# Performance work log

Measured on AMD Instinct MI355X. Metric: run time of the kernel, lower is better.

Reference implementation:

```python
import jax, jax.numpy as jnp
import numpy as np

B, S, H = 2, 2048, 2048
N = 16               # num heads
NOPE, ROPE, V = 128, 64, 128
QHD = NOPE + ROPE    # 192 per-head q/k dim
QL, KVL = 1536, 512  # q_lora_rank, kv_lora_rank
THETA = 10000.0
SCALE = QHD ** -0.5
EPS = 1e-6


def rmsnorm(x, w):
    var = jnp.mean(x.astype(jnp.float32) ** 2, axis=-1, keepdims=True)
    return (x.astype(jnp.float32) * jax.lax.rsqrt(var + EPS)).astype(x.dtype) * w


def rotate_half(x):
    d = x.shape[-1] // 2
    return jnp.concatenate([-x[..., d:], x[..., :d]], axis=-1)


def setup_inputs() -> dict:
    key = jax.random.key(0)
    ks = jax.random.split(key, 8)
    w = lambda k, shape: jax.random.normal(k, shape, jnp.float32) * 0.02
    return {
        "hidden_states": jax.random.normal(ks[0], (B, S, H), jnp.float32),
        "position_ids": (jnp.arange(B * S, dtype=jnp.int64) % 4096).reshape(B, S),
        "q_a_w": w(ks[1], (QL, H)),
        "q_a_ln_w": jnp.ones((QL,), jnp.float32),
        "q_b_w": w(ks[2], (N * QHD, QL)),
        "kv_a_w": w(ks[3], (KVL + ROPE, H)),
        "kv_a_ln_w": jnp.ones((KVL,), jnp.float32),
        "kv_b_w": w(ks[4], (N * (NOPE + V), KVL)),
        "o_w": w(ks[5], (H, N * V)),
    }


def mla_forward(hidden_states, position_ids, q_a_w, q_a_ln_w, q_b_w,
                kv_a_w, kv_a_ln_w, kv_b_w, o_w):
    b, s, _ = hidden_states.shape
    # ---- Q low-rank path: q_b(rmsnorm(q_a(x))) ----
    q = rmsnorm(hidden_states @ q_a_w.T, q_a_ln_w) @ q_b_w.T
    q = q.reshape(b, s, N, QHD)
    q_nope, q_pe = q[..., :NOPE], q[..., NOPE:]
    # ---- compressed KV + shared rope key ----
    kv_a = hidden_states @ kv_a_w.T                       # [b,s,KVL+ROPE]
    compressed_kv = rmsnorm(kv_a[..., :KVL], kv_a_ln_w)   # [b,s,KVL]
    k_pe = kv_a[..., KVL:].reshape(b, s, 1, ROPE)         # MQA rope key
    # ---- RoPE (default, theta=1e4) from position_ids ----
    inv_freq = 1.0 / (THETA ** (jnp.arange(0, ROPE, 2, dtype=jnp.float32) / ROPE))
    freqs = position_ids.astype(jnp.float32)[..., None] * inv_freq  # [b,s,ROPE/2]
    emb = jnp.concatenate([freqs, freqs], axis=-1)                  # [b,s,ROPE]
    cos = jnp.cos(emb)[:, :, None, :].astype(hidden_states.dtype)   # [b,s,1,ROPE]
    sin = jnp.sin(emb)[:, :, None, :].astype(hidden_states.dtype)
    q_pe = q_pe * cos + rotate_half(q_pe) * sin
    k_pe = k_pe * cos + rotate_half(k_pe) * sin
    # ---- decompress latent KV via kv_b_proj ----
    kv = (compressed_kv @ kv_b_w.T).reshape(b, s, N, NOPE + V)
    k_nope, v = kv[..., :NOPE], kv[..., NOPE:]
    k = jnp.concatenate([k_nope, jnp.broadcast_to(k_pe, (b, s, N, ROPE))], axis=-1)
    qf = jnp.concatenate([q_nope, q_pe], axis=-1)          # [b,s,N,QHD]
    # ---- causal SDPA in bsnd layout ----
    scores = jnp.einsum('bqnd,bknd->bnqk', qf, k) * SCALE  # [b,N,s,s]
    causal = jnp.tril(jnp.ones((s, s), bool))
    scores = jnp.where(causal, scores, jnp.finfo(scores.dtype).min)
    probs = jax.nn.softmax(scores, axis=-1)
    attn = jnp.einsum('bnqk,bknd->bqnd', probs, v)         # [b,s,N,V]
    out = attn.reshape(b, s, N * V) @ o_w.T
    return out


def reference(hidden_states, position_ids, q_a_w, q_a_ln_w, q_b_w,
              kv_a_w, kv_a_ln_w, kv_b_w, o_w):
    return mla_forward(hidden_states, position_ids, q_a_w, q_a_ln_w, q_b_w,
                       kv_a_w, kv_a_ln_w, kv_b_w, o_w)
```

## Files before the change

### kernel.cpp

```cpp
#include <hip/hip_runtime.h>
#include <cstdio>

typedef unsigned short u16;
typedef u16 u16x4 __attribute__((ext_vector_type(4)));
typedef u16 u16x8 __attribute__((ext_vector_type(8)));
typedef __bf16 bf16x8 __attribute__((ext_vector_type(8)));
typedef float f32x4 __attribute__((ext_vector_type(4)));

#define AS1 __attribute__((address_space(1)))
#define AS3 __attribute__((address_space(3)))

#define GLOAD16(gsrc, ldst) __builtin_amdgcn_global_load_lds( \
    (const AS1 void*)(gsrc), (AS3 void*)(ldst), 16, 0, 0)

__device__ __forceinline__ u16 f2bf(float f) {
  unsigned u = __builtin_bit_cast(unsigned, f);
  u += 0x7fffu + ((u >> 16) & 1u);
  return (u16)(u >> 16);
}
__device__ __forceinline__ float bf2f(u16 h) {
  return __builtin_bit_cast(float, (unsigned)h << 16);
}

__global__ __launch_bounds__(256) void cvt_pad_k(const float* __restrict__ src,
                                                 u16* __restrict__ dst,
                                                 long srcN, long dstN) {
  long i = ((long)blockIdx.x * 256 + threadIdx.x) * 8;
  const long stride = (long)gridDim.x * 256 * 8;
  for (; i < dstN; i += stride) {
    u16x8 o = {0,0,0,0,0,0,0,0};
    if (i < srcN) {
      const float4* p = (const float4*)(src + i);
      float4 a = p[0], b = p[1];
      o[0]=f2bf(a.x); o[1]=f2bf(a.y); o[2]=f2bf(a.z); o[3]=f2bf(a.w);
      o[4]=f2bf(b.x); o[5]=f2bf(b.y); o[6]=f2bf(b.z); o[7]=f2bf(b.w);
    }
    *(u16x8*)(dst + i) = o;
  }
}

__global__ __launch_bounds__(256) void rms_k(const u16* __restrict__ src, u16* __restrict__ dst,
                                             const float* __restrict__ w,
                                             int sstride, int dstride, int cols) {
  const int row = blockIdx.x;
  const int tid = threadIdx.x;
  const int nch = cols >> 3;
  float x[8];
  float ss = 0.f;
  if (tid < nch) {
    u16x8 v = *(const u16x8*)(src + (size_t)row * sstride + tid * 8);
#pragma unroll
    for (int j = 0; j < 8; ++j) { x[j] = bf2f(v[j]); ss += x[j] * x[j]; }
  } else {
#pragma unroll
    for (int j = 0; j < 8; ++j) x[j] = 0.f;
  }
#pragma unroll
  for (int off = 1; off < 64; off <<= 1) ss += __shfl_xor(ss, off);
  __shared__ float red[4];
  const int wv = tid >> 6, ln = tid & 63;
  if (ln == 0) red[wv] = ss;
  __syncthreads();
  const float tot = red[0] + red[1] + red[2] + red[3];
  const float rs = 1.0f / sqrtf(tot / (float)cols + 1e-6f);
  if (tid < nch) {
    u16x8 o;
#pragma unroll
    for (int j = 0; j < 8; ++j) o[j] = f2bf(x[j] * rs * w[tid * 8 + j]);
    *(u16x8*)(dst + (size_t)row * dstride + tid * 8) = o;
  }
}

__global__ __launch_bounds__(256) void rope_k(u16* __restrict__ q, const u16* __restrict__ kva,
                                              u16* __restrict__ kpe, const int* __restrict__ pos) {
  const int tok = blockIdx.x;
  const int j = threadIdx.x & 63;
  const int w = threadIdx.x >> 6;
  const float p = (float)pos[tok];
  const int jj = j & 31;
  const float inv = __powf(10000.0f, -(float)jj * (1.0f / 32.0f));
  float s, c;
  __sincosf(p * inv, &s, &c);
  const float sgn = (j < 32) ? -1.0f : 1.0f;
  const int partner = (j < 32) ? j + 32 : j - 32;
  if (w == 0) {
    const float x  = bf2f(kva[(size_t)tok * 640 + 512 + j]);
    const float xp = bf2f(kva[(size_t)tok * 640 + 512 + partner]);
    kpe[(size_t)tok * 64 + j] = f2bf(x * c + sgn * xp * s);
  }
#pragma unroll
  for (int hh = 0; hh < 4; ++hh) {
    const int h = w * 4 + hh;
    const size_t base = (size_t)tok * 3072 + h * 192 + 128;
    const float x  = bf2f(q[base + j]);
    const float xp = bf2f(q[base + partner]);
    q[base + j] = f2bf(x * c + sgn * xp * s);
  }
}

__global__ __launch_bounds__(256) void gemm_bt(const u16* __restrict__ A, const u16* __restrict__ B,
                                               u16* __restrict__ Cb, float* __restrict__ Cf,
                                               int M, int N, int K) {
  __shared__ __attribute__((aligned(16))) u16 As[128 * 64];
  __shared__ __attribute__((aligned(16))) u16 Bs[128 * 64];
  const int tid = threadIdx.x;
  const int m0 = blockIdx.y * 128, n0 = blockIdx.x * 128;
  const int w = tid >> 6, lane = tid & 63;
  const int wr = w >> 1, wc = w & 1;
  const int lr = lane & 15, g = lane >> 4;

  f32x4 acc[4][4] = {};

  for (int k0 = 0; k0 < K; k0 += 64) {
#pragma unroll
    for (int i = 0; i < 4; ++i) {
      const int c = i * 256 + tid;
      const int row = c >> 3, col = (c & 7) << 3;
      GLOAD16(A + (size_t)(m0 + row) * K + k0 + col, &As[c * 8]);
    }
#pragma unroll
    for (int i = 0; i < 4; ++i) {
      const int c = i * 256 + tid;
      const int row = c >> 3, col = (c & 7) << 3;
      GLOAD16(B + (size_t)(n0 + row) * K + k0 + col, &Bs[c * 8]);
    }
    __syncthreads();
    bf16x8 af[4][2], bfr[4][2];
#pragma unroll
    for (int x = 0; x < 4; ++x)
#pragma unroll
      for (int kk = 0; kk < 2; ++kk) {
        af[x][kk]  = *(const bf16x8*)(&As[(wr * 64 + x * 16 + lr) * 64 + kk * 32 + g * 8]);
        bfr[x][kk] = *(const bf16x8*)(&Bs[(wc * 64 + x * 16 + lr) * 64 + kk * 32 + g * 8]);
      }
#pragma unroll
    for (int mi = 0; mi < 4; ++mi)
#pragma unroll
      for (int ni = 0; ni < 4; ++ni)
#pragma unroll
        for (int kk = 0; kk < 2; ++kk)
          acc[mi][ni] = __builtin_amdgcn_mfma_f32_16x16x32_bf16(af[mi][kk], bfr[ni][kk],
                                                                acc[mi][ni], 0, 0, 0);
    __syncthreads();
  }

  const int rb = m0 + wr * 64, cb = n0 + wc * 64;
#pragma unroll
  for (int mi = 0; mi < 4; ++mi)
#pragma unroll
    for (int ni = 0; ni < 4; ++ni)
#pragma unroll
      for (int i = 0; i < 4; ++i) {
        const int r = rb + mi * 16 + g * 4 + i;
        const int cI = cb + ni * 16 + lr;
        if (Cf) Cf[(size_t)r * N + cI] = acc[mi][ni][i];
        else    Cb[(size_t)r * N + cI] = f2bf(acc[mi][ni][i]);
      }
}

__global__ __launch_bounds__(256) void attn_k(const u16* __restrict__ q, const u16* __restrict__ kvb,
                                              const u16* __restrict__ kpe, u16* __restrict__ ao) {
  __shared__ __attribute__((aligned(16))) u16 Ks[64 * 192];
  __shared__ __attribute__((aligned(16))) u16 Vt[128 * 64];
  __shared__ __attribute__((aligned(16))) u16 Ps[4][32 * 72];

  const float SCALE = 0.07216878364870323f;
  const int bh = blockIdx.x;
  const int b = bh >> 4, h = bh & 15;
  const int by = blockIdx.y;
  const int j = (by < 8) ? (15 - by) : (by - 8);
  const int tid = threadIdx.x, w = tid >> 6, lane = tid & 63;
  const int lr = lane & 15, g = lane >> 4;

  const int q0 = j * 128;
  const int qrb = q0 + w * 32;

  bf16x8 qf[2][6];
#pragma unroll
  for (int m = 0; m < 2; ++m)
#pragma unroll
    for (int kd = 0; kd < 6; ++kd)
      qf[m][kd] = *(const bf16x8*)(q + (size_t)(b * 2048 + qrb + m * 16 + lr) * 3072 +
                                   h * 192 + kd * 32 + g * 8);

  float mrow[2][4], lrow[2][4];
  f32x4 o[2][8] = {};
#pragma unroll
  for (int m = 0; m < 2; ++m)
#pragma unroll
    for (int i = 0; i < 4; ++i) { mrow[m][i] = -1e30f; lrow[m][i] = 0.f; }

  const int nt = (q0 >> 6) + 2;
  for (int t = 0; t < nt; ++t) {
    const int k0 = t * 64;
#pragma unroll
    for (int i = 0; i < 6; ++i) {
      const int c = i * 256 + tid;
      const int row = c / 24, cl = c - row * 24;
      const int cg = cl ^ (row & 7);
      const u16* src = (cg < 16)
        ? (kvb + (size_t)(b * 2048 + k0 + row) * 4096 + h * 256 + cg * 8)
        : (kpe + (size_t)(b * 2048 + k0 + row) * 64 + (cg - 16) * 8);
      GLOAD16(src, &Ks[c * 8]);
    }
    {
      const int kq = tid >> 4;
      const int vc = (tid & 15) << 3;
      u16x8 vv[4];
#pragma unroll
      for (int r = 0; r < 4; ++r)
        vv[r] = *(const u16x8*)(kvb + (size_t)(b * 2048 + k0 + kq * 4 + r) * 4096 + h * 256 + 128 + vc);
#pragma unroll
      for (int e = 0; e < 8; ++e) {
        const int v = vc + e;
        const int cx = (kq >> 1) ^ (v & 7) ^ ((v >> 3) & 7);
        u16x4 tq = {vv[0][e], vv[1][e], vv[2][e], vv[3][e]};
        *(u16x4*)(&Vt[v * 64 + cx * 8 + (kq & 1) * 4]) = tq;
      }
    }
    __syncthreads();

    if (k0 <= qrb + 31) {
      f32x4 sAcc[2][4] = {};
#pragma unroll
      for (int nf = 0; nf < 4; ++nf) {
        const int rr = nf * 16 + lr;
#pragma unroll
        for (int kd = 0; kd < 6; ++kd) {
          const int ch = (kd * 4 + g) ^ (rr & 7);
          const bf16x8 kf = *(const bf16x8*)(&Ks[rr * 192 + ch * 8]);
#pragma unroll
          for (int m = 0; m < 2; ++m)
            sAcc[m][nf] = __builtin_amdgcn_mfma_f32_16x16x32_bf16(qf[m][kd], kf, sAcc[m][nf], 0, 0, 0);
        }
      }

#pragma unroll
      for (int m = 0; m < 2; ++m) {
        float sv[4][4];
#pragma unroll
        for (int nf = 0; nf < 4; ++nf)
#pragma unroll
          for (int i = 0; i < 4; ++i) {
            const int qrow = qrb + m * 16 + g * 4 + i;
            const int kcol = k0 + nf * 16 + lr;
            const float vS = sAcc[m][nf][i] * SCALE;
            sv[nf][i] = (kcol > qrow) ? -1e30f : vS;
          }
        float rm4[4];
        bool exceed = false;
#pragma unroll
        for (int i = 0; i < 4; ++i) {
          float rm = fmaxf(fmaxf(sv[0][i], sv[1][i]), fmaxf(sv[2][i], sv[3][i]));
          rm = fmaxf(rm, __shfl_xor(rm, 1));
          rm = fmaxf(rm, __shfl_xor(rm, 2));
          rm = fmaxf(rm, __shfl_xor(rm, 4));
          rm = fmaxf(rm, __shfl_xor(rm, 8));
          rm4[i] = rm;
          exceed = exceed || (rm > mrow[m][i] + 8.0f);
        }
        if (__any(exceed)) {
#pragma unroll
          for (int i = 0; i < 4; ++i) {
            const float mn = fmaxf(mrow[m][i], rm4[i]);
            const float fac = __expf(mrow[m][i] - mn);
            mrow[m][i] = mn;
            lrow[m][i] *= fac;
#pragma unroll
            for (int nv = 0; nv < 8; ++nv) o[m][nv][i] *= fac;
          }
        }
#pragma unroll
        for (int i = 0; i < 4; ++i) {
          float rsum = 0.f;
#pragma unroll
          for (int nf = 0; nf < 4; ++nf) { sv[nf][i] = __expf(sv[nf][i] - mrow[m][i]); rsum += sv[nf][i]; }
          rsum += __shfl_xor(rsum, 1);
          rsum += __shfl_xor(rsum, 2);
          rsum += __shfl_xor(rsum, 4);
          rsum += __shfl_xor(rsum, 8);
          lrow[m][i] += rsum;
        }
#pragma unroll
        for (int nf = 0; nf < 4; ++nf)
#pragma unroll
          for (int i = 0; i < 4; ++i)
            Ps[w][(m * 16 + g * 4 + i) * 72 + nf * 16 + lr] = f2bf(sv[nf][i]);
      }
      asm volatile("s_waitcnt lgkmcnt(0)" ::: "memory");

#pragma unroll
      for (int kc = 0; kc < 2; ++kc) {
        bf16x8 vfr[8];
#pragma unroll
        for (int nv = 0; nv < 8; ++nv) {
          const int v = nv * 16 + lr;
          const int cx = (kc * 4 + g) ^ (v & 7) ^ ((v >> 3) & 7);
          vfr[nv] = *(const bf16x8*)(&Vt[v * 64 + cx * 8]);
        }
#pragma unroll
        for (int m = 0; m < 2; ++m) {
          const bf16x8 pf = *(const bf16x8*)(&Ps[w][(m * 16 + lr) * 72 + kc * 32 + g * 8]);
#pragma unroll
          for (int nv = 0; nv < 8; ++nv)
            o[m][nv] = __builtin_amdgcn_mfma_f32_16x16x32_bf16(pf, vfr[nv], o[m][nv], 0, 0, 0);
        }
      }
    }
    __syncthreads();
  }

#pragma unroll
  for (int m = 0; m < 2; ++m)
#pragma unroll
    for (int i = 0; i < 4; ++i) {
      const float inv = 1.0f / lrow[m][i];
      const size_t tokOff = (size_t)(b * 2048 + qrb + m * 16 + g * 4 + i) * 2048 + h * 128;
#pragma unroll
      for (int nv = 0; nv < 8; ++nv)
        ao[tokOff + nv * 16 + lr] = f2bf(o[m][nv][i] * inv);
    }
}

extern "C" void kernel_launch(void* const* d_in, const int* in_sizes, int n_in,
                              void* d_out, int out_size, void* d_ws, size_t ws_size,
                              hipStream_t stream) {
  const float* hidden  = (const float*)d_in[0];
  const int*   pos     = (const int*)d_in[1];
  const float* q_a_w   = (const float*)d_in[2];
  const float* q_a_ln  = (const float*)d_in[3];
  const float* q_b_w   = (const float*)d_in[4];
  const float* kv_a_w  = (const float*)d_in[5];
  const float* kv_a_ln = (const float*)d_in[6];
  const float* kv_b_w  = (const float*)d_in[7];
  const float* o_w     = (const float*)d_in[8];
  float* out = (float*)d_out;

  char* ws = (char*)d_ws;
  u16* hb  = (u16*)(ws + 0L);
  u16* w1  = (u16*)(ws + 16777216L);
  u16* w2  = (u16*)(ws + 23068672L);
  u16* w3  = (u16*)(ws + 32505856L);
  u16* w4  = (u16*)(ws + 35127296L);
  u16* w5  = (u16*)(ws + 39321600L);
  u16* qa  = (u16*)(ws + 47710208L);
  u16* qb  = (u16*)(ws + 60293120L);
  u16* kva = (u16*)(ws + 85458944L);
  u16* ckv = (u16*)(ws + 90701824L);
  u16* kpe = (u16*)(ws + 94896128L);
  u16* kvb = (u16*)(ws + 95420416L);
  u16* ao  = (u16*)(ws + 128974848L);
  if (ws_size < 145752064UL) { fprintf(stderr, "ws too small: %zu\n", ws_size); return; }

  auto cvt = [&](const float* s, u16* d, long sn, long dn) {
    long blocks = (dn / 8 + 255) / 256; if (blocks > 2048) blocks = 2048;
    cvt_pad_k<<<dim3((unsigned)blocks), dim3(256), 0, stream>>>(s, d, sn, dn);
  };
  cvt(hidden, hb, 4096L * 2048, 4096L * 2048);
  cvt(q_a_w,  w1, 1536L * 2048, 1536L * 2048);
  cvt(q_b_w,  w2, 3072L * 1536, 3072L * 1536);
  cvt(kv_a_w, w3, 576L * 2048,  640L * 2048);
  cvt(kv_b_w, w4, 4096L * 512,  4096L * 512);
  cvt(o_w,    w5, 2048L * 2048, 2048L * 2048);

  gemm_bt<<<dim3(12, 32), 256, 0, stream>>>(hb, w1, qa, nullptr, 4096, 1536, 2048);
  rms_k<<<4096, 256, 0, stream>>>(qa, qa, q_a_ln, 1536, 1536, 1536);
  gemm_bt<<<dim3(24, 32), 256, 0, stream>>>(qa, w2, qb, nullptr, 4096, 3072, 1536);
  gemm_bt<<<dim3(5, 32), 256, 0, stream>>>(hb, w3, kva, nullptr, 4096, 640, 2048);
  rms_k<<<4096, 256, 0, stream>>>(kva, ckv, kv_a_ln, 640, 512, 512);
  rope_k<<<4096, 256, 0, stream>>>(qb, kva, kpe, pos);
  gemm_bt<<<dim3(32, 32), 256, 0, stream>>>(ckv, w4, kvb, nullptr, 4096, 4096, 512);
  attn_k<<<dim3(32, 16), 256, 0, stream>>>(qb, kvb, kpe, ao);
  gemm_bt<<<dim3(16, 32), 256, 0, stream>>>(ao, w5, nullptr, out, 4096, 2048, 2048);
}
```

Measured before the change: 503.2 us.

## Fuse q_a/kv_a GEMMs, write transposed V from kv_b GEMM, fold scale into Q

Concatenates the q_a and kv_a weights so a single GEMM produces both low-rank projections. The kv_b GEMM epilogue now writes V pre-transposed into a per-head buffer, so attention can load K and V with async global-to-LDS copies and skips the register transpose. The softmax scale moves into the q_b GEMM epilogue, and causal masking runs only on diagonal tiles. The change also adds s_setprio around the MFMA sections, uses precomputed load offsets, and drops the interleaved block ordering. The risks are the strided transposed-V stores in the GEMM epilogue and reuse of workspace buffers (vT aliases hb, qk_a aliases kvb).

```diff
diff --git a/kernel.cpp b/kernel.cpp
--- a/kernel.cpp
+++ b/kernel.cpp
@@ -71,7 +71,7 @@
   }
 }
 
-__global__ __launch_bounds__(256) void rope_k(u16* __restrict__ q, const u16* __restrict__ kva,
+__global__ __launch_bounds__(256) void rope_k(u16* __restrict__ q, const u16* __restrict__ qk_a,
                                               u16* __restrict__ kpe, const int* __restrict__ pos) {
   const int tok = blockIdx.x;
   const int j = threadIdx.x & 63;
@@ -84,8 +84,8 @@
   const float sgn = (j < 32) ? -1.0f : 1.0f;
   const int partner = (j < 32) ? j + 32 : j - 32;
   if (w == 0) {
-    const float x  = bf2f(kva[(size_t)tok * 640 + 512 + j]);
-    const float xp = bf2f(kva[(size_t)tok * 640 + 512 + partner]);
+    const float x  = bf2f(qk_a[(size_t)tok * 2176 + 2048 + j]);
+    const float xp = bf2f(qk_a[(size_t)tok * 2176 + 2048 + partner]);
     kpe[(size_t)tok * 64 + j] = f2bf(x * c + sgn * xp * s);
   }
 #pragma unroll
@@ -100,7 +100,8 @@
 
 __global__ __launch_bounds__(256) void gemm_bt(const u16* __restrict__ A, const u16* __restrict__ B,
                                                u16* __restrict__ Cb, float* __restrict__ Cf,
-                                               int M, int N, int K) {
+                                               int M, int N, int K, float cs,
+                                               u16* __restrict__ vTr) {
   __shared__ __attribute__((aligned(16))) u16 As[128 * 64];
   __shared__ __attribute__((aligned(16))) u16 Bs[128 * 64];
   const int tid = threadIdx.x;
@@ -148,32 +149,69 @@
 #pragma unroll
   for (int mi = 0; mi < 4; ++mi)
 #pragma unroll
-    for (int ni = 0; ni < 4; ++ni)
-#pragma unroll
-      for (int i = 0; i < 4; ++i) {
-        const int r = rb + mi * 16 + g * 4 + i;
-        const int cI = cb + ni * 16 + lr;
-        if (Cf) Cf[(size_t)r * N + cI] = acc[mi][ni][i];
-        else    Cb[(size_t)r * N + cI] = f2bf(acc[mi][ni][i]);
+    for (int ni = 0; ni < 4; ++ni) {
+      const int r = rb + mi * 16 + g * 4;
+      const int cI = cb + ni * 16 + lr;
+      if (vTr) {
+        const u16 v0 = f2bf(acc[mi][ni][0]), v1 = f2bf(acc[mi][ni][1]);
+        const u16 v2 = f2bf(acc[mi][ni][2]), v3 = f2bf(acc[mi][ni][3]);
+        if ((cI & 255) < 128) {
+          Cb[(size_t)(r + 0) * N + cI] = v0;
+          Cb[(size_t)(r + 1) * N + cI] = v1;
+          Cb[(size_t)(r + 2) * N + cI] = v2;
+          Cb[(size_t)(r + 3) * N + cI] = v3;
+        } else {
+          u16x4 tq = {v0, v1, v2, v3};
+          const int bh = ((r >> 11) << 4) + (cI >> 8);
+          *(u16x4*)(vTr + (size_t)(bh * 128 + (cI & 127)) * 2048 + (r & 2047)) = tq;
+        }
+      } else {
+#pragma unroll
+        for (int i = 0; i < 4; ++i) {
+          if (Cf) Cf[(size_t)(r + i) * N + cI] = acc[mi][ni][i] * cs;
+          else    Cb[(size_t)(r + i) * N + cI] = f2bf(acc[mi][ni][i] * cs);
+        }
       }
-}
-
-__global__ __launch_bounds__(256) void attn_k(const u16* __restrict__ q, const u16* __restrict__ kvb,
-                                              const u16* __restrict__ kpe, u16* __restrict__ ao) {
+    }
+}
+
+__global__ __launch_bounds__(256) void attn_k(const u16* __restrict__ q, const u16* __restrict__ kpe,
+                                              const u16* __restrict__ vT, u16* __restrict__ ao) {
   __shared__ __attribute__((aligned(16))) u16 Ks[64 * 192];
   __shared__ __attribute__((aligned(16))) u16 Vt[128 * 64];
   __shared__ __attribute__((aligned(16))) u16 Ps[4][32 * 72];
 
-  const float SCALE = 0.07216878364870323f;
   const int bh = blockIdx.x;
   const int b = bh >> 4, h = bh & 15;
-  const int by = blockIdx.y;
-  const int j = (by < 8) ? (15 - by) : (by - 8);
+  const int j = 15 - blockIdx.y;
   const int tid = threadIdx.x, w = tid >> 6, lane = tid & 63;
   const int lr = lane & 15, g = lane >> 4;
 
   const int q0 = j * 128;
   const int qrb = q0 + w * 32;
+  u16* Psw = &Ps[w][0];
+
+  int koff[6], kstep[6], kld[6];
+#pragma unroll
+  for (int i = 0; i < 6; ++i) {
+    const int c = i * 256 + tid;
+    const int row = c / 24, cl = c - row * 24;
+    const int cg = cl ^ (row & 7);
+    kld[i] = c * 8;
+    if (cg < 16) { koff[i] = 262144 + (b * 2048 + row) * 4096 + h * 256 + cg * 8;
+                   kstep[i] = 64 * 4096; }
+    else         { koff[i] = (b * 2048 + row) * 64 + (cg - 16) * 8;
+                   kstep[i] = 64 * 64; }
+  }
+  int voff[4], vld[4];
+#pragma unroll
+  for (int i = 0; i < 4; ++i) {
+    const int c = i * 256 + tid;
+    const int v = c >> 3, cl = c & 7;
+    const int cg = cl ^ (v & 7);
+    vld[i] = c * 8;
+    voff[i] = (bh * 128 + v) * 2048 + cg * 8;
+  }
 
   bf16x8 qf[2][6];
 #pragma unroll
@@ -195,33 +233,20 @@
     const int k0 = t * 64;
 #pragma unroll
     for (int i = 0; i < 6; ++i) {
-      const int c = i * 256 + tid;
-      const int row = c / 24, cl = c - row * 24;
-      const int cg = cl ^ (row & 7);
-      const u16* src = (cg < 16)
-        ? (kvb + (size_t)(b * 2048 + k0 + row) * 4096 + h * 256 + cg * 8)
-        : (kpe + (size_t)(b * 2048 + k0 + row) * 64 + (cg - 16) * 8);
-      GLOAD16(src, &Ks[c * 8]);
-    }
-    {
-      const int kq = tid >> 4;
-      const int vc = (tid & 15) << 3;
-      u16x8 vv[4];
-#pragma unroll
-      for (int r = 0; r < 4; ++r)
-        vv[r] = *(const u16x8*)(kvb + (size_t)(b * 2048 + k0 + kq * 4 + r) * 4096 + h * 256 + 128 + vc);
-#pragma unroll
-      for (int e = 0; e < 8; ++e) {
-        const int v = vc + e;
-        const int cx = (kq >> 1) ^ (v & 7) ^ ((v >> 3) & 7);
-        u16x4 tq = {vv[0][e], vv[1][e], vv[2][e], vv[3][e]};
-        *(u16x4*)(&Vt[v * 64 + cx * 8 + (kq & 1) * 4]) = tq;
-      }
+      GLOAD16(kpe + koff[i], &Ks[kld[i]]);
+      koff[i] += kstep[i];
+    }
+#pragma unroll
+    for (int i = 0; i < 4; ++i) {
+      GLOAD16(vT + voff[i], &Vt[vld[i]]);
+      voff[i] += 64;
     }
     __syncthreads();
 
-    if (k0 <= qrb + 31) {
+    const bool active = (k0 <= qrb + 31);
+    if (active) {
       f32x4 sAcc[2][4] = {};
+      __builtin_amdgcn_s_setprio(1);
 #pragma unroll
       for (int nf = 0; nf < 4; ++nf) {
         const int rr = nf * 16 + lr;
@@ -234,19 +259,27 @@
             sAcc[m][nf] = __builtin_amdgcn_mfma_f32_16x16x32_bf16(qf[m][kd], kf, sAcc[m][nf], 0, 0, 0);
         }
       }
-
+      __builtin_amdgcn_s_setprio(0);
+
+      const bool needMask = (k0 + 63 > qrb);
 #pragma unroll
       for (int m = 0; m < 2; ++m) {
         float sv[4][4];
-#pragma unroll
-        for (int nf = 0; nf < 4; ++nf)
-#pragma unroll
-          for (int i = 0; i < 4; ++i) {
-            const int qrow = qrb + m * 16 + g * 4 + i;
-            const int kcol = k0 + nf * 16 + lr;
-            const float vS = sAcc[m][nf][i] * SCALE;
-            sv[nf][i] = (kcol > qrow) ? -1e30f : vS;
-          }
+        if (needMask) {
+#pragma unroll
+          for (int nf = 0; nf < 4; ++nf)
+#pragma unroll
+            for (int i = 0; i < 4; ++i) {
+              const int qrow = qrb + m * 16 + g * 4 + i;
+              const int kcol = k0 + nf * 16 + lr;
+              sv[nf][i] = (kcol > qrow) ? -1e30f : sAcc[m][nf][i];
+            }
+        } else {
+#pragma unroll
+          for (int nf = 0; nf < 4; ++nf)
+#pragma unroll
+            for (int i = 0; i < 4; ++i) sv[nf][i] = sAcc[m][nf][i];
+        }
         float rm4[4];
         bool exceed = false;
 #pragma unroll
@@ -285,27 +318,29 @@
         for (int nf = 0; nf < 4; ++nf)
 #pragma unroll
           for (int i = 0; i < 4; ++i)
-            Ps[w][(m * 16 + g * 4 + i) * 72 + nf * 16 + lr] = f2bf(sv[nf][i]);
+            Psw[(m * 16 + g * 4 + i) * 72 + nf * 16 + lr] = f2bf(sv[nf][i]);
       }
       asm volatile("s_waitcnt lgkmcnt(0)" ::: "memory");
 
+      __builtin_amdgcn_s_setprio(1);
 #pragma unroll
       for (int kc = 0; kc < 2; ++kc) {
         bf16x8 vfr[8];
 #pragma unroll
         for (int nv = 0; nv < 8; ++nv) {
           const int v = nv * 16 + lr;
-          const int cx = (kc * 4 + g) ^ (v & 7) ^ ((v >> 3) & 7);
+          const int cx = (kc * 4 + g) ^ (v & 7);
           vfr[nv] = *(const bf16x8*)(&Vt[v * 64 + cx * 8]);
         }
 #pragma unroll
         for (int m = 0; m < 2; ++m) {
-          const bf16x8 pf = *(const bf16x8*)(&Ps[w][(m * 16 + lr) * 72 + kc * 32 + g * 8]);
+          const bf16x8 pf = *(const bf16x8*)(&Psw[(m * 16 + lr) * 72 + kc * 32 + g * 8]);
 #pragma unroll
           for (int nv = 0; nv < 8; ++nv)
             o[m][nv] = __builtin_amdgcn_mfma_f32_16x16x32_bf16(pf, vfr[nv], o[m][nv], 0, 0, 0);
         }
       }
+      __builtin_amdgcn_s_setprio(0);
     }
     __syncthreads();
   }
@@ -338,38 +373,39 @@
 
   char* ws = (char*)d_ws;
   u16* hb  = (u16*)(ws + 0L);
-  u16* w1  = (u16*)(ws + 16777216L);
-  u16* w2  = (u16*)(ws + 23068672L);
-  u16* w3  = (u16*)(ws + 32505856L);
+  u16* wA  = (u16*)(ws + 16777216L);
+  u16* w2  = (u16*)(ws + 25690112L);
   u16* w4  = (u16*)(ws + 35127296L);
   u16* w5  = (u16*)(ws + 39321600L);
   u16* qa  = (u16*)(ws + 47710208L);
   u16* qb  = (u16*)(ws + 60293120L);
-  u16* kva = (u16*)(ws + 85458944L);
-  u16* ckv = (u16*)(ws + 90701824L);
-  u16* kpe = (u16*)(ws + 94896128L);
-  u16* kvb = (u16*)(ws + 95420416L);
-  u16* ao  = (u16*)(ws + 128974848L);
+  u16* ckv = (u16*)(ws + 85458944L);
+  u16* kpe = (u16*)(ws + 89653248L);
+  u16* kvb = (u16*)(ws + 90177536L);
+  u16* ao  = (u16*)(ws + 123731968L);
+  u16* qk_a = kvb;
+  u16* vT  = hb;
   if (ws_size < 145752064UL) { fprintf(stderr, "ws too small: %zu\n", ws_size); return; }
+
+  const float SCALE = 0.07216878364870323f;
 
   auto cvt = [&](const float* s, u16* d, long sn, long dn) {
     long blocks = (dn / 8 + 255) / 256; if (blocks > 2048) blocks = 2048;
     cvt_pad_k<<<dim3((unsigned)blocks), dim3(256), 0, stream>>>(s, d, sn, dn);
   };
   cvt(hidden, hb, 4096L * 2048, 4096L * 2048);
-  cvt(q_a_w,  w1, 1536L * 2048, 1536L * 2048);
+  cvt(q_a_w,  wA, 1536L * 2048, 1536L * 2048);
+  cvt(kv_a_w, wA + 1536L * 2048, 576L * 2048, 640L * 2048);
   cvt(q_b_w,  w2, 3072L * 1536, 3072L * 1536);
-  cvt(kv_a_w, w3, 576L * 2048,  640L * 2048);
   cvt(kv_b_w, w4, 4096L * 512,  4096L * 512);
   cvt(o_w,    w5, 2048L * 2048, 2048L * 2048);
 
-  gemm_bt<<<dim3(12, 32), 256, 0, stream>>>(hb, w1, qa, nullptr, 4096, 1536, 2048);
-  rms_k<<<4096, 256, 0, stream>>>(qa, qa, q_a_ln, 1536, 1536, 1536);
-  gemm_bt<<<dim3(24, 32), 256, 0, stream>>>(qa, w2, qb, nullptr, 4096, 3072, 1536);
-  gemm_bt<<<dim3(5, 32), 256, 0, stream>>>(hb, w3, kva, nullptr, 4096, 640, 2048);
-  rms_k<<<4096, 256, 0, stream>>>(kva, ckv, kv_a_ln, 640, 512, 512);
-  rope_k<<<4096, 256, 0, stream>>>(qb, kva, kpe, pos);
-  gemm_bt<<<dim3(32, 32), 256, 0, stream>>>(ckv, w4, kvb, nullptr, 4096, 4096, 512);
-  attn_k<<<dim3(32, 16), 256, 0, stream>>>(qb, kvb, kpe, ao);
-  gemm_bt<<<dim3(16, 32), 256, 0, stream>>>(ao, w5, nullptr, out, 4096, 2048, 2048);
-}
+  gemm_bt<<<dim3(17, 32), 256, 0, stream>>>(hb, wA, qk_a, nullptr, 4096, 2176, 2048, 1.0f, nullptr);
+  rms_k<<<4096, 256, 0, stream>>>(qk_a, qa, q_a_ln, 2176, 1536, 1536);
+  rms_k<<<4096, 256, 0, stream>>>(qk_a + 1536, ckv, kv_a_ln, 2176, 512, 512);
+  gemm_bt<<<dim3(24, 32), 256, 0, stream>>>(qa, w2, qb, nullptr, 4096, 3072, 1536, SCALE, nullptr);
+  rope_k<<<4096, 256, 0, stream>>>(qb, qk_a, kpe, pos);
+  gemm_bt<<<dim3(32, 32), 256, 0, stream>>>(ckv, w4, kvb, nullptr, 4096, 4096, 512, 1.0f, vT);
+  attn_k<<<dim3(32, 16), 256, 0, stream>>>(qb, kpe, vT, ao);
+  gemm_bt<<<dim3(16, 32), 256, 0, stream>>>(ao, w5, nullptr, out, 4096, 2048, 2048, 1.0f, nullptr);
+}
```

Measured after the change: 423.3 us. 15.9% less time.
